# Kernel tuning notes

Measured on AMD Instinct MI355X. Metric: run time of the kernel, lower is better.

Reference implementation:

```python
import jax, jax.numpy as jnp
import numpy as np

V, E, D, B, C = 100000, 256, 128, 8192, 10  # vocab, embedding_size, context_size, batch, window


def setup_inputs() -> dict:
    key = jax.random.key(0)
    ks = jax.random.split(key, 11)
    s = 0.02
    return {
        "x": jax.random.randint(ks[0], (B,), 0, V),
        "context": jax.random.randint(ks[1], (B, C), 0, V),
        "W_emb": jax.random.normal(ks[2], (V, E), jnp.float32) * s,
        "M_w": jax.random.normal(ks[3], (D, E), jnp.float32) * s,
        "M_b": jnp.zeros((D,), jnp.float32),
        "U_w": jax.random.normal(ks[4], (D, 2 * D), jnp.float32) * s,
        "U_b": jnp.zeros((D,), jnp.float32),
        "W_w": jax.random.normal(ks[5], (D, 2 * D), jnp.float32) * s,
        "W_b": jnp.zeros((D,), jnp.float32),
        "prior_mus": jax.random.normal(ks[6], (V, D), jnp.float32) * s,
        # covariance diagonal must be positive for a valid Gaussian (torch would
        # Cholesky-fail otherwise); sample in [0.1, 1.0)
        "prior_sigmas": jax.random.uniform(ks[7], (V, D), jnp.float32, 0.1, 1.0),
    }


def reference(x, context, W_emb, M_w, M_b, U_w, U_b, W_w, W_b, prior_mus, prior_sigmas):
    emb_x = W_emb[x]                       # [B, E]
    emb_c = W_emb[context]                 # [B, C, E]
    Rw = emb_x @ M_w.T + M_b               # [B, D]  (repeated over C slots below)
    Rc = jnp.einsum('bce,de->bcd', emb_c, M_w) + M_b  # [B, C, D]
    RwC = jnp.broadcast_to(Rw[:, None, :], Rc.shape)   # repeat(len(context), 1)
    h = jax.nn.relu(jnp.concatenate([RwC, Rc], axis=-1)).sum(axis=1)  # [B, 2D]
    mu = h @ U_w.T + U_b                   # posterior mean  [B, D]
    sigma = jax.nn.softplus(h @ W_w.T + W_b)  # posterior cov diag [B, D]
    m0 = prior_mus[x]                      # prior mean      [B, D]
    s0 = prior_sigmas[x]                   # prior cov diag  [B, D]
    # closed-form KL(N(m0, diag(s0)) || N(mu, diag(sigma)))
    d = jnp.float32(D)
    kl = 0.5 * ((s0 / sigma).sum(-1)
                + ((mu - m0) ** 2 / sigma).sum(-1)
                - d
                + jnp.log(sigma).sum(-1) - jnp.log(s0).sum(-1))
    return kl  # [B]
```

## Files before the change

kernel.cpp:

```cpp
#include <hip/hip_runtime.h>
#include <hip/hip_bf16.h>
#include <math.h>


#define CTXN  10
#define DDIM  128
#define WS_M   0
#define WS_UW  32768

#define BT    16
#define ROWSP 192
#define LP    72
#define ACH   (ROWSP * LP)
#define HLP   264
#define XLP   132

typedef short bf16x8 __attribute__((ext_vector_type(8)));
typedef float f32x4  __attribute__((ext_vector_type(4)));

__device__ __forceinline__ uint2 cvt4(float4 v) {
    union { __hip_bfloat162 h2; unsigned u; } a, b;
    a.h2 = __float22bfloat162_rn(make_float2(v.x, v.y));
    b.h2 = __float22bfloat162_rn(make_float2(v.z, v.w));
    return make_uint2(a.u, b.u);
}

__device__ __forceinline__ float softplusf(float v) {
    return fmaxf(v, 0.0f) + log1pf(expf(-fabsf(v)));
}

__global__ __launch_bounds__(256) void k_cvt(
    const float* __restrict__ M_w, const float* __restrict__ U_w,
    const float* __restrict__ W_w, unsigned short* __restrict__ ws)
{
    int which = blockIdx.x >> 5;
    int i = ((blockIdx.x & 31) << 8) | threadIdx.x;
    const float* src = (which == 0) ? M_w : (which == 1) ? U_w : W_w;
    float4 v = ((const float4*)src)[i];
    *(uint2*)&ws[which * 32768 + i * 4] = cvt4(v);
}

__global__ __launch_bounds__(1024, 2) void bsg_one(
    const int* __restrict__ x, const int* __restrict__ ctx,
    const float* __restrict__ W_emb, const float* __restrict__ M_b,
    const float* __restrict__ U_b,   const float* __restrict__ W_b,
    const float* __restrict__ pmu,   const float* __restrict__ psg,
    const unsigned short* __restrict__ wsr, float* __restrict__ out)
{
    __shared__ __align__(16) unsigned short A_s[2 * ACH];
    __shared__ __align__(16) unsigned short H_s[BT * HLP];
    __shared__ int   idx_s[ROWSP];
    __shared__ float P_s[BT * 8];

    const int tid  = threadIdx.x;
    const int b0   = blockIdx.x * BT;
    const int w    = tid >> 6;
    const int n    = w & 7;
    const int mg   = w >> 3;
    const int lane = tid & 63;
    const int l15  = lane & 15;
    const int lg   = lane >> 4;

    if (tid < ROWSP) {
        int c = tid >> 4, b = b0 + (tid & 15);
        idx_s[tid] = (c >= 11) ? 0 : ((c == 0) ? x[b] : ctx[b * CTXN + (c - 1)]);
    }
    __syncthreads();

    const int r0 = tid >> 4, q0 = tid & 15;
    const int r1 = r0 + 64;
    const int r2 = r0 + 128;

    float4 rr0[3], rr1[3];
    const float4* We = (const float4*)W_emb;
#define LOADC(dst, ch)                                                          \
    {                                                                           \
        dst[0] = We[(size_t)idx_s[r0] * 64 + (ch) * 16 + q0];                   \
        dst[1] = We[(size_t)idx_s[r1] * 64 + (ch) * 16 + q0];                   \
        dst[2] = We[(size_t)idx_s[r2] * 64 + (ch) * 16 + q0];                   \
    }
#define WRITEC(Ab, src)                                                         \
    {                                                                           \
        *(uint2*)&(Ab)[r0 * LP + 4 * q0] = cvt4(src[0]);                        \
        *(uint2*)&(Ab)[r1 * LP + 4 * q0] = cvt4(src[1]);                        \
        *(uint2*)&(Ab)[r2 * LP + 4 * q0] = cvt4(src[2]);                        \
    }

    LOADC(rr0, 0);
    LOADC(rr1, 1);

    const unsigned short* Mb_bf = wsr + WS_M;
    const int mrow = 16 * n + l15;
    f32x4 acc[6] = {};

#pragma unroll
    for (int ch = 0; ch < 4; ++ch) {
        unsigned short* Ab = A_s + (ch & 1) * ACH;
        if (ch & 1) { WRITEC(Ab, rr1); if (ch < 2) LOADC(rr1, ch + 2); }
        else        { WRITEC(Ab, rr0); if (ch < 2) LOADC(rr0, ch + 2); }
        __syncthreads();
        bf16x8 m0 = *(const bf16x8*)&Mb_bf[mrow * 256 + 64 * ch + 8 * lg];
        bf16x8 m1 = *(const bf16x8*)&Mb_bf[mrow * 256 + 64 * ch + 32 + 8 * lg];
        const unsigned short* Abr = A_s + (ch & 1) * ACH;
#pragma unroll
        for (int mt = 0; mt < 6; ++mt) {
            if (mg == 0 || mt < 5) {
                int tile = 6 * mg + mt;
                bf16x8 a0 = *(const bf16x8*)&Abr[(16 * tile + l15) * LP + 8 * lg];
                bf16x8 a1 = *(const bf16x8*)&Abr[(16 * tile + l15) * LP + 32 + 8 * lg];
                acc[mt] = __builtin_amdgcn_mfma_f32_16x16x32_bf16(a0, m0, acc[mt], 0, 0, 0);
                acc[mt] = __builtin_amdgcn_mfma_f32_16x16x32_bf16(a1, m1, acc[mt], 0, 0, 0);
            }
        }
    }
#undef LOADC
#undef WRITEC

    const int dg = 16 * n + l15;
    const float mb = M_b[dg];
    float* X_s = (float*)A_s;

    if (mg == 1) {
#pragma unroll
        for (int q = 0; q < 4; ++q) {
            float s = 0.0f;
#pragma unroll
            for (int mt = 0; mt < 5; ++mt) s += fmaxf(acc[mt][q] + mb, 0.0f);
            X_s[(4 * lg + q) * XLP + dg] = s;
        }
    }
    __syncthreads();

    if (mg == 0) {
#pragma unroll
        for (int q = 0; q < 4; ++q) {
            float h1 = 10.0f * fmaxf(acc[0][q] + mb, 0.0f);
            float s  = 0.0f;
#pragma unroll
            for (int mt = 1; mt < 6; ++mt) s += fmaxf(acc[mt][q] + mb, 0.0f);
            s += X_s[(4 * lg + q) * XLP + dg];
            int b = 4 * lg + q;
            __hip_bfloat16 t1 = __float2bfloat16(h1);
            __hip_bfloat16 t2 = __float2bfloat16(s);
            H_s[b * HLP + dg]       = *(unsigned short*)&t1;
            H_s[b * HLP + 128 + dg] = *(unsigned short*)&t2;
        }
    }

    float pm[4], ps[4];
    if (w < 8) {
#pragma unroll
        for (int q = 0; q < 4; ++q) {
            int xb = idx_s[4 * lg + q];
            pm[q] = pmu[(size_t)xb * DDIM + dg];
            ps[q] = psg[(size_t)xb * DDIM + dg];
        }
    }
    __syncthreads();

    if (w < 8) {
        const unsigned short* UWb = wsr + WS_UW;
        f32x4 acc2[2] = {};
#pragma unroll
        for (int ks = 0; ks < 8; ++ks) {
            bf16x8 hf = *(const bf16x8*)&H_s[l15 * HLP + 32 * ks + 8 * lg];
            bf16x8 bu = *(const bf16x8*)&UWb[dg * 256 + 32 * ks + 8 * lg];
            bf16x8 bw = *(const bf16x8*)&UWb[(128 + dg) * 256 + 32 * ks + 8 * lg];
            acc2[0] = __builtin_amdgcn_mfma_f32_16x16x32_bf16(hf, bu, acc2[0], 0, 0, 0);
            acc2[1] = __builtin_amdgcn_mfma_f32_16x16x32_bf16(hf, bw, acc2[1], 0, 0, 0);
        }
        const float ub = U_b[dg], wb = W_b[dg];
#pragma unroll
        for (int q = 0; q < 4; ++q) {
            int rb = 4 * lg + q;
            float mu = acc2[0][q] + ub;
            float sg = softplusf(acc2[1][q] + wb);
            float dm = mu - pm[q];
            float p  = ps[q] / sg + dm * dm / sg + logf(sg) - logf(ps[q]);
            p += __shfl_xor(p, 1);
            p += __shfl_xor(p, 2);
            p += __shfl_xor(p, 4);
            p += __shfl_xor(p, 8);
            if (l15 == 0) P_s[rb * 8 + w] = p;
        }
    }
    __syncthreads();
    if (tid < BT) {
        float s = 0.0f;
#pragma unroll
        for (int k = 0; k < 8; ++k) s += P_s[tid * 8 + k];
        out[b0 + tid] = 0.5f * (s - (float)DDIM);
    }
}

extern "C" void kernel_launch(void* const* d_in, const int* in_sizes, int n_in,
                              void* d_out, int out_size, void* d_ws, size_t ws_size,
                              hipStream_t stream) {
    const int*   x     = (const int*)  d_in[0];
    const int*   ctx   = (const int*)  d_in[1];
    const float* W_emb = (const float*)d_in[2];
    const float* M_w   = (const float*)d_in[3];
    const float* M_b   = (const float*)d_in[4];
    const float* U_w   = (const float*)d_in[5];
    const float* U_b   = (const float*)d_in[6];
    const float* W_w   = (const float*)d_in[7];
    const float* W_b   = (const float*)d_in[8];
    const float* pmu   = (const float*)d_in[9];
    const float* psg   = (const float*)d_in[10];
    float* out = (float*)d_out;
    unsigned short* ws = (unsigned short*)d_ws;

    k_cvt<<<dim3(96), dim3(256), 0, stream>>>(M_w, U_w, W_w, ws);
    bsg_one<<<dim3(8192 / BT), dim3(1024), 0, stream>>>(
        x, ctx, W_emb, M_b, U_b, W_b, pmu, psg, ws, out);
}
```

Baseline: 46.43 us.

## Give each wave one embedding-row tile and load prior stats in spare waves

Each of 11 waves now owns 16 gathered embedding rows and computes all 128 output columns. Rows are loaded straight from global into registers and converted to bf16 fragments, so the shared-memory A staging and the per-chunk barriers are gone. The ReLU outputs are stored as bf16 in shared memory and reduced over the context slots by all threads. The remaining 5 waves prefetch prior means and sigmas into shared memory while the MFMAs run. This trades less LDS staging and fewer barriers for more global reads of the M weights per wave, plus an extra bf16 rounding of the intermediate ReLU values before the sum.

```diff
diff --git a/kernel.cpp b/kernel.cpp
--- a/kernel.cpp
+++ b/kernel.cpp
@@ -9,11 +9,8 @@
 #define WS_UW  32768
 
 #define BT    16
-#define ROWSP 192
-#define LP    72
-#define ACH   (ROWSP * LP)
+#define RLP   136
 #define HLP   264
-#define XLP   132
 
 typedef short bf16x8 __attribute__((ext_vector_type(8)));
 typedef float f32x4  __attribute__((ext_vector_type(4)));
@@ -23,6 +20,19 @@
     a.h2 = __float22bfloat162_rn(make_float2(v.x, v.y));
     b.h2 = __float22bfloat162_rn(make_float2(v.z, v.w));
     return make_uint2(a.u, b.u);
+}
+
+__device__ __forceinline__ bf16x8 cvt8(float4 a, float4 b) {
+    union { __hip_bfloat162 h2[4]; bf16x8 v; } u;
+    u.h2[0] = __float22bfloat162_rn(make_float2(a.x, a.y));
+    u.h2[1] = __float22bfloat162_rn(make_float2(a.z, a.w));
+    u.h2[2] = __float22bfloat162_rn(make_float2(b.x, b.y));
+    u.h2[3] = __float22bfloat162_rn(make_float2(b.z, b.w));
+    return u.v;
+}
+
+__device__ __forceinline__ float bf2f(unsigned short s) {
+    union { unsigned u; float f; } t; t.u = (unsigned)s << 16; return t.f;
 }
 
 __device__ __forceinline__ float softplusf(float v) {
@@ -40,125 +50,94 @@
     *(uint2*)&ws[which * 32768 + i * 4] = cvt4(v);
 }
 
-__global__ __launch_bounds__(1024, 2) void bsg_one(
+__global__ __launch_bounds__(1024, 8) void bsg_one(
     const int* __restrict__ x, const int* __restrict__ ctx,
     const float* __restrict__ W_emb, const float* __restrict__ M_b,
     const float* __restrict__ U_b,   const float* __restrict__ W_b,
     const float* __restrict__ pmu,   const float* __restrict__ psg,
     const unsigned short* __restrict__ wsr, float* __restrict__ out)
 {
-    __shared__ __align__(16) unsigned short A_s[2 * ACH];
+    __shared__ __align__(16) unsigned short R_s[176 * RLP];
     __shared__ __align__(16) unsigned short H_s[BT * HLP];
-    __shared__ int   idx_s[ROWSP];
+    __shared__ float pm_s[BT * DDIM];
+    __shared__ float ps_s[BT * DDIM];
+    __shared__ float Mb_s[DDIM];
+    __shared__ int   idx_s[176];
     __shared__ float P_s[BT * 8];
 
     const int tid  = threadIdx.x;
     const int b0   = blockIdx.x * BT;
     const int w    = tid >> 6;
-    const int n    = w & 7;
-    const int mg   = w >> 3;
     const int lane = tid & 63;
     const int l15  = lane & 15;
     const int lg   = lane >> 4;
 
-    if (tid < ROWSP) {
+    if (tid < 176) {
         int c = tid >> 4, b = b0 + (tid & 15);
-        idx_s[tid] = (c >= 11) ? 0 : ((c == 0) ? x[b] : ctx[b * CTXN + (c - 1)]);
+        idx_s[tid] = (c == 0) ? x[b] : ctx[b * CTXN + (c - 1)];
     }
+    if (tid < DDIM) Mb_s[tid] = M_b[tid];
     __syncthreads();
 
-    const int r0 = tid >> 4, q0 = tid & 15;
-    const int r1 = r0 + 64;
-    const int r2 = r0 + 128;
-
-    float4 rr0[3], rr1[3];
-    const float4* We = (const float4*)W_emb;
-#define LOADC(dst, ch)                                                          \
-    {                                                                           \
-        dst[0] = We[(size_t)idx_s[r0] * 64 + (ch) * 16 + q0];                   \
-        dst[1] = We[(size_t)idx_s[r1] * 64 + (ch) * 16 + q0];                   \
-        dst[2] = We[(size_t)idx_s[r2] * 64 + (ch) * 16 + q0];                   \
-    }
-#define WRITEC(Ab, src)                                                         \
-    {                                                                           \
-        *(uint2*)&(Ab)[r0 * LP + 4 * q0] = cvt4(src[0]);                        \
-        *(uint2*)&(Ab)[r1 * LP + 4 * q0] = cvt4(src[1]);                        \
-        *(uint2*)&(Ab)[r2 * LP + 4 * q0] = cvt4(src[2]);                        \
-    }
-
-    LOADC(rr0, 0);
-    LOADC(rr1, 1);
-
-    const unsigned short* Mb_bf = wsr + WS_M;
-    const int mrow = 16 * n + l15;
-    f32x4 acc[6] = {};
-
+    if (w < 11) {
+        const size_t base = (size_t)idx_s[16 * w + l15] * 64;
+        const float4* We = (const float4*)W_emb;
+        const unsigned short* Mb_bf = wsr + WS_M;
+        f32x4 acc[8] = {};
+        float4 a0 = We[base + 2 * lg];
+        float4 a1 = We[base + 2 * lg + 1];
 #pragma unroll
-    for (int ch = 0; ch < 4; ++ch) {
-        unsigned short* Ab = A_s + (ch & 1) * ACH;
-        if (ch & 1) { WRITEC(Ab, rr1); if (ch < 2) LOADC(rr1, ch + 2); }
-        else        { WRITEC(Ab, rr0); if (ch < 2) LOADC(rr0, ch + 2); }
-        __syncthreads();
-        bf16x8 m0 = *(const bf16x8*)&Mb_bf[mrow * 256 + 64 * ch + 8 * lg];
-        bf16x8 m1 = *(const bf16x8*)&Mb_bf[mrow * 256 + 64 * ch + 32 + 8 * lg];
-        const unsigned short* Abr = A_s + (ch & 1) * ACH;
+        for (int ch = 0; ch < 8; ++ch) {
+            bf16x8 af = cvt8(a0, a1);
+            if (ch < 7) {
+                a0 = We[base + 8 * (ch + 1) + 2 * lg];
+                a1 = We[base + 8 * (ch + 1) + 2 * lg + 1];
+            }
 #pragma unroll
-        for (int mt = 0; mt < 6; ++mt) {
-            if (mg == 0 || mt < 5) {
-                int tile = 6 * mg + mt;
-                bf16x8 a0 = *(const bf16x8*)&Abr[(16 * tile + l15) * LP + 8 * lg];
-                bf16x8 a1 = *(const bf16x8*)&Abr[(16 * tile + l15) * LP + 32 + 8 * lg];
-                acc[mt] = __builtin_amdgcn_mfma_f32_16x16x32_bf16(a0, m0, acc[mt], 0, 0, 0);
-                acc[mt] = __builtin_amdgcn_mfma_f32_16x16x32_bf16(a1, m1, acc[mt], 0, 0, 0);
+            for (int nt = 0; nt < 8; ++nt) {
+                bf16x8 bf = *(const bf16x8*)&Mb_bf[(16 * nt + l15) * 256 + 32 * ch + 8 * lg];
+                acc[nt] = __builtin_amdgcn_mfma_f32_16x16x32_bf16(af, bf, acc[nt], 0, 0, 0);
             }
         }
-    }
-#undef LOADC
-#undef WRITEC
-
-    const int dg = 16 * n + l15;
-    const float mb = M_b[dg];
-    float* X_s = (float*)A_s;
-
-    if (mg == 1) {
 #pragma unroll
-        for (int q = 0; q < 4; ++q) {
-            float s = 0.0f;
+        for (int nt = 0; nt < 8; ++nt) {
+            int d = 16 * nt + l15;
+            float mb = Mb_s[d];
 #pragma unroll
-            for (int mt = 0; mt < 5; ++mt) s += fmaxf(acc[mt][q] + mb, 0.0f);
-            X_s[(4 * lg + q) * XLP + dg] = s;
+            for (int q = 0; q < 4; ++q) {
+                float r = fmaxf(acc[nt][q] + mb, 0.0f);
+                __hip_bfloat16 t = __float2bfloat16(r);
+                R_s[(16 * w + 4 * lg + q) * RLP + d] = *(unsigned short*)&t;
+            }
+        }
+    } else {
+        int hid = tid - 704;
+        for (int v = hid; v < BT * DDIM; v += 320) {
+            int b = v >> 7, d = v & 127;
+            int xb = idx_s[b];
+            pm_s[v] = pmu[(size_t)xb * DDIM + d];
+            ps_s[v] = psg[(size_t)xb * DDIM + d];
         }
     }
     __syncthreads();
 
-    if (mg == 0) {
 #pragma unroll
-        for (int q = 0; q < 4; ++q) {
-            float h1 = 10.0f * fmaxf(acc[0][q] + mb, 0.0f);
-            float s  = 0.0f;
+    for (int s = 0; s < 2; ++s) {
+        int p = tid + 1024 * s;
+        int b = p >> 7, d = p & 127;
+        float h1 = 10.0f * bf2f(R_s[b * RLP + d]);
+        float h2 = 0.0f;
 #pragma unroll
-            for (int mt = 1; mt < 6; ++mt) s += fmaxf(acc[mt][q] + mb, 0.0f);
-            s += X_s[(4 * lg + q) * XLP + dg];
-            int b = 4 * lg + q;
-            __hip_bfloat16 t1 = __float2bfloat16(h1);
-            __hip_bfloat16 t2 = __float2bfloat16(s);
-            H_s[b * HLP + dg]       = *(unsigned short*)&t1;
-            H_s[b * HLP + 128 + dg] = *(unsigned short*)&t2;
-        }
-    }
-
-    float pm[4], ps[4];
-    if (w < 8) {
-#pragma unroll
-        for (int q = 0; q < 4; ++q) {
-            int xb = idx_s[4 * lg + q];
-            pm[q] = pmu[(size_t)xb * DDIM + dg];
-            ps[q] = psg[(size_t)xb * DDIM + dg];
-        }
+        for (int c = 1; c < 11; ++c) h2 += bf2f(R_s[(16 * c + b) * RLP + d]);
+        __hip_bfloat16 t1 = __float2bfloat16(h1);
+        __hip_bfloat16 t2 = __float2bfloat16(h2);
+        H_s[b * HLP + d]       = *(unsigned short*)&t1;
+        H_s[b * HLP + 128 + d] = *(unsigned short*)&t2;
     }
     __syncthreads();
 
     if (w < 8) {
+        const int dg = 16 * w + l15;
         const unsigned short* UWb = wsr + WS_UW;
         f32x4 acc2[2] = {};
 #pragma unroll
@@ -175,8 +154,10 @@
             int rb = 4 * lg + q;
             float mu = acc2[0][q] + ub;
             float sg = softplusf(acc2[1][q] + wb);
-            float dm = mu - pm[q];
-            float p  = ps[q] / sg + dm * dm / sg + logf(sg) - logf(ps[q]);
+            float m0 = pm_s[rb * DDIM + dg];
+            float s0 = ps_s[rb * DDIM + dg];
+            float dm = mu - m0;
+            float p  = s0 / sg + dm * dm / sg + logf(sg) - logf(s0);
             p += __shfl_xor(p, 1);
             p += __shfl_xor(p, 2);
             p += __shfl_xor(p, 4);
```

After: 74.02 us. 59.4% more time.
